# Performance work log

Measured on AMD Instinct MI355X. Metric: run time of the kernel, lower is better.

The kernel has to match this reference:

```python
import jax, jax.numpy as jnp
import numpy as np

B, S, E, H = 4, 8192, 512, 8
D = E // H  # head_dim = 64


def setup_inputs() -> dict:
    key = jax.random.key(0)
    ks = jax.random.split(key, 9)
    scale = 1.0 / np.sqrt(E)
    x = jax.random.normal(ks[0], (B, S, E), dtype=jnp.float32)
    # torch nn.Linear convention: y = x @ W.T + b, W has shape (out, in)
    Wp = jax.random.uniform(ks[1], (E, E), jnp.float32, -scale, scale)
    bp = jax.random.uniform(ks[2], (E,), jnp.float32, -scale, scale)
    Wc = jax.random.uniform(ks[3], (E, E), jnp.float32, -scale, scale)
    bc = jax.random.uniform(ks[4], (E,), jnp.float32, -scale, scale)
    Ws = jax.random.uniform(ks[5], (E, E), jnp.float32, -scale, scale)
    bs = jax.random.uniform(ks[6], (E,), jnp.float32, -scale, scale)
    Wo = jax.random.uniform(ks[7], (E, E), jnp.float32, -scale, scale)
    bo = jax.random.uniform(ks[8], (E,), jnp.float32, -scale, scale)
    return {"x": x, "Wp": Wp, "bp": bp, "Wc": Wc, "bc": bc,
            "Ws": Ws, "bs": bs, "Wo": Wo, "bo": bo}


def reference(x, Wp, bp, Wc, bc, Ws, bs, Wo, bo):
    # Faithful to TreeAttention.forward with tree_structure=None (default path).
    # NOTE: original views projections as (B,S,H,D) without transposing head/seq,
    # so the matmuls mix HEADS per token (HxH scores), not tokens.
    b, s, _ = x.shape
    parent = (jnp.einsum('bse,fe->bsf', x, Wp) + bp).reshape(b, s, H, D)
    child = (jnp.einsum('bse,fe->bsf', x, Wc) + bc).reshape(b, s, H, D)
    sibling = (jnp.einsum('bse,fe->bsf', x, Ws) + bs).reshape(b, s, H, D)
    # per-token head-mixing scores: (B, S, H, H)
    scores = jnp.einsum('bshd,bstd->bsht', parent, child) / jnp.sqrt(
        jnp.asarray(D, dtype=x.dtype))
    attention = jax.nn.softmax(scores, axis=-1)
    # dropout is identity in eval mode (reference runs in inference mode)
    out = jnp.einsum('bsht,bstd->bshd', attention, sibling).reshape(b, s, E)
    return jnp.einsum('bse,fe->bsf', out, Wo) + bo
```

## Files before the change

### kernel.cpp

```cpp
#include <hip/hip_runtime.h>
#include <hip/hip_bf16.h>

typedef unsigned short u16;
typedef __attribute__((ext_vector_type(8))) short bf16x8;
typedef __attribute__((ext_vector_type(4))) float f32x4;
typedef __attribute__((ext_vector_type(8))) unsigned short u16x8;

#define GLDS(gp, lp) __builtin_amdgcn_global_load_lds( \
    (const __attribute__((address_space(1))) void*)(gp), \
    (__attribute__((address_space(3))) void*)(lp), 16, 0, 0)

__device__ __forceinline__ u16 f2b(float f) {
  unsigned u = __builtin_bit_cast(unsigned, f);
  return (u16)((u + 0x7fffu + ((u >> 16) & 1u)) >> 16);
}
__device__ __forceinline__ float b2f(u16 s) {
  return __builtin_bit_cast(float, (unsigned)s << 16);
}

#define BARX() do { __builtin_amdgcn_sched_barrier(0); \
  asm volatile("s_barrier" ::: "memory"); \
  __builtin_amdgcn_sched_barrier(0); } while (0)

__global__ __launch_bounds__(256) void convert_k(
    const float* __restrict__ x, const float* __restrict__ Wp,
    const float* __restrict__ Wc, const float* __restrict__ Ws,
    const float* __restrict__ Wo, u16* __restrict__ xb,
    u16* __restrict__ wall, u16* __restrict__ wob)
{
  const long CX = 2097152;
  const long CW = 98304;
  const long CO = 32768;
  const long total = CX + CW + CO;
  for (long i = (long)blockIdx.x * blockDim.x + threadIdx.x; i < total;
       i += (long)gridDim.x * blockDim.x) {
    const float* src; u16* dst;
    if (i < CX) {
      src = x + i * 8; dst = xb + i * 8;
    } else if (i < CX + CW) {
      long e = (i - CX) * 8;
      int n = (int)(e >> 9), k = (int)(e & 511);
      const float* wr = (n < 512)  ? (Wp + (long)n * 512)
                      : (n < 1024) ? (Wc + (long)(n - 512) * 512)
                                   : (Ws + (long)(n - 1024) * 512);
      src = wr + k; dst = wall + e;
    } else {
      long e = (i - CX - CW) * 8; src = Wo + e; dst = wob + e;
    }
    f32x4 v0 = *(const f32x4*)src;
    f32x4 v1 = *(const f32x4*)(src + 4);
    u16x8 o;
    o[0]=f2b(v0[0]); o[1]=f2b(v0[1]); o[2]=f2b(v0[2]); o[3]=f2b(v0[3]);
    o[4]=f2b(v1[0]); o[5]=f2b(v1[1]); o[6]=f2b(v1[2]); o[7]=f2b(v1[3]);
    *(u16x8*)dst = o;
  }
}

template<int NC, bool BF16OUT>
__global__ __launch_bounds__(512, 2) void gemm8(
    const u16* __restrict__ A, const u16* __restrict__ Bw,
    const float* __restrict__ bias0, const float* __restrict__ bias1,
    const float* __restrict__ bias2, void* __restrict__ Cout)
{
  __shared__ alignas(16) char smem[131072];
  char* sAc = smem;
  char* sBc = smem + 65536;

  const int tid = threadIdx.x;
  const int w = tid >> 6, lane = tid & 63;
  const int wr = w >> 2, wc = w & 3;
  const int ln15 = lane & 15, g4 = lane >> 4, l7 = lane & 7;

  const int nbx = NC / 256;
  const int nwg = nbx * 128;
  const int qq = nwg / 8;
  const int flat = blockIdx.x;
  const int swz = (flat & 7) * qq + (flat >> 3);
  const int bx = swz % nbx, by = swz / nbx;
  const long row0 = (long)by * 256;
  const int col0 = bx * 256;

  const int t8 = tid >> 3;
  const int gsw = (tid & 7) ^ (t8 & 7);
  const u16* pA = A + (row0 + t8) * 512 + gsw * 8;
  const u16* pB = Bw + ((long)col0 + (t8 >> 5) * 64 + (t8 & 31)) * 512 + gsw * 8;

#define STG_A(bb, h, t) do { \
    const u16* s_ = pA + (h) * 32768 + (t) * 64; \
    char* d_ = sAc + (bb) * 32768 + (h) * 16384 + w * 1024; \
    GLDS(s_, d_); GLDS(s_ + 65536, d_ + 8192); \
  } while (0)
#define STG_B(bb, h, t) do { \
    const u16* s_ = pB + (h) * 16384 + (t) * 64; \
    char* d_ = sBc + (bb) * 32768 + (h) * 16384 + w * 1024; \
    GLDS(s_, d_); GLDS(s_ + 65536, d_ + 8192); \
  } while (0)

  const int gkb0 = (g4 ^ l7) << 4;
  const int gkb1 = ((g4 + 4) ^ l7) << 4;
  const int aoff = (wr * 64 + ln15) * 128;
  const int boff = (wc * 32 + ln15) * 128;

#define LOAD_A(bb, MH) do { \
    const char* ba_ = sAc + (bb) * 32768 + (MH) * 16384 + aoff; \
    _Pragma("unroll") for (int mf = 0; mf < 4; ++mf) { \
      aF[mf][0] = *(const bf16x8*)(ba_ + mf * 2048 + gkb0); \
      aF[mf][1] = *(const bf16x8*)(ba_ + mf * 2048 + gkb1); \
    } } while (0)
#define LOAD_B(bb, NH, BF) do { \
    const char* bb_ = sBc + (bb) * 32768 + (NH) * 16384 + boff; \
    _Pragma("unroll") for (int nf = 0; nf < 2; ++nf) { \
      BF[nf][0] = *(const bf16x8*)(bb_ + nf * 2048 + gkb0); \
      BF[nf][1] = *(const bf16x8*)(bb_ + nf * 2048 + gkb1); \
    } } while (0)
#define MFMA_Q(MH, NH, BF) do { \
    __builtin_amdgcn_s_setprio(1); \
    _Pragma("unroll") for (int mf = 0; mf < 4; ++mf) \
    _Pragma("unroll") for (int nf = 0; nf < 2; ++nf) { \
      f32x4 c_ = acc[(MH) * 4 + mf][(NH) * 2 + nf]; \
      c_ = __builtin_amdgcn_mfma_f32_16x16x32_bf16(aF[mf][0], BF[nf][0], c_, 0, 0, 0); \
      c_ = __builtin_amdgcn_mfma_f32_16x16x32_bf16(aF[mf][1], BF[nf][1], c_, 0, 0, 0); \
      acc[(MH) * 4 + mf][(NH) * 2 + nf] = c_; \
    } \
    __builtin_amdgcn_s_setprio(0); \
  } while (0)
#define WAITB(nstr) do { \
    asm volatile("s_waitcnt vmcnt(" nstr ")" ::: "memory"); BARX(); } while (0)

  f32x4 acc[8][4] = {};

  STG_A(0, 0, 0); STG_B(0, 0, 0); STG_B(0, 1, 0); STG_A(0, 1, 0);
  STG_A(1, 0, 1); STG_B(1, 0, 1); STG_B(1, 1, 1);
  WAITB("10");

#pragma unroll
  for (int it = 0; it < 4; ++it) {
    const int t0 = 2 * it, t1 = t0 + 1;
    const bool st = (it < 3);
    bf16x8 aF[4][2], bFa[2][2], bFb[2][2];

    LOAD_A(0, 0); LOAD_B(0, 0, bFa);
    STG_A(1, 1, t1);
    MFMA_Q(0, 0, bFa);
    if (st) WAITB("10"); else WAITB("2");
    LOAD_B(0, 1, bFb);
    if (st) STG_A(0, 0, t0 + 2);
    MFMA_Q(0, 1, bFb);
    if (st) WAITB("10"); else WAITB("2");
    LOAD_A(0, 1);
    if (st) STG_B(0, 0, t0 + 2);
    MFMA_Q(1, 1, bFb);
    if (st) WAITB("10"); else WAITB("2");
    if (st) STG_B(0, 1, t0 + 2);
    MFMA_Q(1, 0, bFa);
    if (st) WAITB("10"); else WAITB("2");
    LOAD_A(1, 0); LOAD_B(1, 0, bFa);
    if (st) STG_A(0, 1, t0 + 2);
    MFMA_Q(0, 0, bFa);
    if (st) WAITB("10"); else WAITB("2");
    LOAD_B(1, 1, bFb);
    if (st) STG_A(1, 0, t1 + 2);
    MFMA_Q(0, 1, bFb);
    if (st) WAITB("10"); else WAITB("0");
    LOAD_A(1, 1);
    if (st) STG_B(1, 0, t1 + 2);
    MFMA_Q(1, 1, bFb);
    if (st) WAITB("10"); else WAITB("0");
    if (st) STG_B(1, 1, t1 + 2);
    MFMA_Q(1, 0, bFa);
    if (st) WAITB("10"); else WAITB("0");
  }

  __syncthreads();
  const long rgb = row0 + wr * 128;
  const int cgb = col0 + wc * 64;
  if (BF16OUT) {
    u16* sc = (u16*)(smem + (w << 14));
#pragma unroll
    for (int n = 0; n < 4; ++n) {
      const int colg = cgb + ln15 + n * 16;
      const float* bp_ = (NC == 512) ? bias0
                         : (colg < 512 ? bias0 : (colg < 1024 ? bias1 : bias2));
      const float bv = bp_[colg & 511];
      const int c = ln15 + n * 16;
      const int gsl = c >> 3, co = c & 7;
#pragma unroll
      for (int mi = 0; mi < 8; ++mi)
#pragma unroll
        for (int j = 0; j < 4; ++j) {
          const int r = mi * 16 + (g4 << 2) + j;
          sc[r * 64 + (((gsl ^ (r & 7)) << 3) | co)] = f2b(acc[mi][n][j] + bv);
        }
    }
    asm volatile("s_waitcnt lgkmcnt(0)" ::: "memory");
    __builtin_amdgcn_sched_barrier(0);
#pragma unroll
    for (int it = 0; it < 16; ++it) {
      const int rr = it * 8 + (lane >> 3);
      const int gl = lane & 7;
      u16x8 v = *(const u16x8*)(sc + rr * 64 + ((gl ^ (rr & 7)) << 3));
      *(u16x8*)((u16*)Cout + (rgb + rr) * NC + cgb + gl * 8) = v;
    }
  } else {
    float* scf = (float*)(smem + (w << 14));
#pragma unroll
    for (int h = 0; h < 2; ++h) {
#pragma unroll
      for (int n = 0; n < 4; ++n) {
        const int colg = cgb + ln15 + n * 16;
        const float bv = bias0[colg & 511];
        const int c = ln15 + n * 16;
        const int gsl = c >> 2, co = c & 3;
#pragma unroll
        for (int mf = 0; mf < 4; ++mf)
#pragma unroll
          for (int j = 0; j < 4; ++j) {
            const int r = mf * 16 + (g4 << 2) + j;
            scf[r * 64 + (((gsl ^ (r & 7)) << 2) | co)] = acc[h * 4 + mf][n][j] + bv;
          }
      }
      asm volatile("s_waitcnt lgkmcnt(0)" ::: "memory");
      __builtin_amdgcn_sched_barrier(0);
#pragma unroll
      for (int it = 0; it < 16; ++it) {
        const int rr = it * 4 + (lane >> 4);
        const int gl = lane & 15;
        f32x4 v = *(const f32x4*)(scf + rr * 64 + ((gl ^ (rr & 7)) << 2));
        *(f32x4*)((float*)Cout + (rgb + h * 64 + rr) * NC + cgb + gl * 4) = v;
      }
      asm volatile("s_waitcnt lgkmcnt(0)" ::: "memory");
      __builtin_amdgcn_sched_barrier(0);
    }
  }
#undef STG_A
#undef STG_B
#undef LOAD_A
#undef LOAD_B
#undef MFMA_Q
#undef WAITB
}

__global__ __launch_bounds__(256) void attn_k(const u16* __restrict__ PCS,
                                              u16* __restrict__ OUT)
{
  __shared__ float L[4][1664];
  const int w = threadIdx.x >> 6, lane = threadIdx.x & 63;
  const long token = (long)blockIdx.x * 4 + w;
  float* Lw = L[w];
  const int C0 = 544, S0 = 1088, AT0 = 1600;
  const u16* rowp = PCS + token * 1536;
#pragma unroll
  for (int q = 0; q < 3; ++q) {
    u16x8 v = *(const u16x8*)(rowp + q * 512 + lane * 8);
    float* dst = (q < 2) ? (Lw + q * 544 + (lane >> 3) * 68 + (lane & 7) * 8)
                         : (Lw + S0 + lane * 8);
    f32x4 a = {b2f(v[0]), b2f(v[1]), b2f(v[2]), b2f(v[3])};
    f32x4 b = {b2f(v[4]), b2f(v[5]), b2f(v[6]), b2f(v[7])};
    *(f32x4*)dst = a;
    *(f32x4*)(dst + 4) = b;
  }
  const int h = lane >> 3, t = lane & 7;
  float sc = 0.f;
#pragma unroll
  for (int d = 0; d < 64; d += 4) {
    f32x4 pv = *(const f32x4*)(Lw + h * 68 + d);
    f32x4 cv = *(const f32x4*)(Lw + C0 + t * 68 + d);
    sc += pv[0]*cv[0] + pv[1]*cv[1] + pv[2]*cv[2] + pv[3]*cv[3];
  }
  sc *= 0.125f;
  float mx = sc;
  mx = fmaxf(mx, __shfl_xor(mx, 1));
  mx = fmaxf(mx, __shfl_xor(mx, 2));
  mx = fmaxf(mx, __shfl_xor(mx, 4));
  float e = __expf(sc - mx);
  float sm = e;
  sm += __shfl_xor(sm, 1);
  sm += __shfl_xor(sm, 2);
  sm += __shfl_xor(sm, 4);
  Lw[AT0 + lane] = e / sm;
  float o[8] = {0, 0, 0, 0, 0, 0, 0, 0};
#pragma unroll
  for (int tt = 0; tt < 8; ++tt) {
    const float av = Lw[AT0 + h * 8 + tt];
    f32x4 s0 = *(const f32x4*)(Lw + S0 + tt * 64 + t * 8);
    f32x4 s1 = *(const f32x4*)(Lw + S0 + tt * 64 + t * 8 + 4);
    o[0] += av * s0[0]; o[1] += av * s0[1]; o[2] += av * s0[2]; o[3] += av * s0[3];
    o[4] += av * s1[0]; o[5] += av * s1[1]; o[6] += av * s1[2]; o[7] += av * s1[3];
  }
  u16x8 ov;
#pragma unroll
  for (int j = 0; j < 8; ++j) ov[j] = f2b(o[j]);
  *(u16x8*)(OUT + token * 512 + lane * 8) = ov;
}

extern "C" void kernel_launch(void* const* d_in, const int* in_sizes, int n_in,
                              void* d_out, int out_size, void* d_ws, size_t ws_size,
                              hipStream_t stream) {
  const float* x  = (const float*)d_in[0];
  const float* Wp = (const float*)d_in[1];
  const float* bp = (const float*)d_in[2];
  const float* Wc = (const float*)d_in[3];
  const float* bc = (const float*)d_in[4];
  const float* Ws = (const float*)d_in[5];
  const float* bs = (const float*)d_in[6];
  const float* Wo = (const float*)d_in[7];
  const float* bo = (const float*)d_in[8];

  char* ws = (char*)d_ws;
  u16* xb   = (u16*)ws;
  u16* wall = (u16*)(ws + 33554432);
  u16* wob  = (u16*)(ws + 35127296);
  u16* pcs  = (u16*)(ws + 35651584);
  u16* outb = xb;

  convert_k<<<2048, 256, 0, stream>>>(x, Wp, Wc, Ws, Wo, xb, wall, wob);
  gemm8<1536, true><<<768, 512, 0, stream>>>(xb, wall, bp, bc, bs, pcs);
  attn_k<<<8192, 256, 0, stream>>>(pcs, outb);
  gemm8<512, false><<<256, 512, 0, stream>>>(outb, wob, bo, bo, bo, d_out);
}
```

Baseline: 136.5 us.

## Halve GEMM LDS to single-buffered stages with in-place refill pipeline

Shrinks the GEMM's shared memory from 128KB to 64KB by dropping the double-buffered K stage and refilling each A/B half in place right after it is consumed, with a rewritten wait/barrier schedule. The epilogue is split into smaller row chunks so it fits the smaller per-wave scratch area. The intent is to allow two 512-thread workgroups per CU, matching the launch bounds, so memory latency is hidden by occupancy rather than by buffering. The trade-off is less prefetch distance inside each block and more barriers per K step.

```diff
diff --git a/kernel.cpp b/kernel.cpp
--- a/kernel.cpp
+++ b/kernel.cpp
@@ -62,9 +62,9 @@
     const float* __restrict__ bias0, const float* __restrict__ bias1,
     const float* __restrict__ bias2, void* __restrict__ Cout)
 {
-  __shared__ alignas(16) char smem[131072];
+  __shared__ alignas(16) char smem[65536];
   char* sAc = smem;
-  char* sBc = smem + 65536;
+  char* sBc = smem + 32768;
 
   const int tid = threadIdx.x;
   const int w = tid >> 6, lane = tid & 63;
@@ -85,14 +85,14 @@
   const u16* pA = A + (row0 + t8) * 512 + gsw * 8;
   const u16* pB = Bw + ((long)col0 + (t8 >> 5) * 64 + (t8 & 31)) * 512 + gsw * 8;
 
-#define STG_A(bb, h, t) do { \
+#define STG_A(h, t) do { \
     const u16* s_ = pA + (h) * 32768 + (t) * 64; \
-    char* d_ = sAc + (bb) * 32768 + (h) * 16384 + w * 1024; \
+    char* d_ = sAc + (h) * 16384 + w * 1024; \
     GLDS(s_, d_); GLDS(s_ + 65536, d_ + 8192); \
   } while (0)
-#define STG_B(bb, h, t) do { \
+#define STG_B(h, t) do { \
     const u16* s_ = pB + (h) * 16384 + (t) * 64; \
-    char* d_ = sBc + (bb) * 32768 + (h) * 16384 + w * 1024; \
+    char* d_ = sBc + (h) * 16384 + w * 1024; \
     GLDS(s_, d_); GLDS(s_ + 65536, d_ + 8192); \
   } while (0)
 
@@ -101,14 +101,14 @@
   const int aoff = (wr * 64 + ln15) * 128;
   const int boff = (wc * 32 + ln15) * 128;
 
-#define LOAD_A(bb, MH) do { \
-    const char* ba_ = sAc + (bb) * 32768 + (MH) * 16384 + aoff; \
+#define LOAD_A(MH) do { \
+    const char* ba_ = sAc + (MH) * 16384 + aoff; \
     _Pragma("unroll") for (int mf = 0; mf < 4; ++mf) { \
       aF[mf][0] = *(const bf16x8*)(ba_ + mf * 2048 + gkb0); \
       aF[mf][1] = *(const bf16x8*)(ba_ + mf * 2048 + gkb1); \
     } } while (0)
-#define LOAD_B(bb, NH, BF) do { \
-    const char* bb_ = sBc + (bb) * 32768 + (NH) * 16384 + boff; \
+#define LOAD_B(NH, BF) do { \
+    const char* bb_ = sBc + (NH) * 16384 + boff; \
     _Pragma("unroll") for (int nf = 0; nf < 2; ++nf) { \
       BF[nf][0] = *(const bf16x8*)(bb_ + nf * 2048 + gkb0); \
       BF[nf][1] = *(const bf16x8*)(bb_ + nf * 2048 + gkb1); \
@@ -124,87 +124,72 @@
     } \
     __builtin_amdgcn_s_setprio(0); \
   } while (0)
-#define WAITB(nstr) do { \
-    asm volatile("s_waitcnt vmcnt(" nstr ")" ::: "memory"); BARX(); } while (0)
+#define VMW(nstr) asm volatile("s_waitcnt vmcnt(" nstr ")" ::: "memory")
 
   f32x4 acc[8][4] = {};
 
-  STG_A(0, 0, 0); STG_B(0, 0, 0); STG_B(0, 1, 0); STG_A(0, 1, 0);
-  STG_A(1, 0, 1); STG_B(1, 0, 1); STG_B(1, 1, 1);
-  WAITB("10");
-
-#pragma unroll
-  for (int it = 0; it < 4; ++it) {
-    const int t0 = 2 * it, t1 = t0 + 1;
-    const bool st = (it < 3);
+  STG_A(0, 0); STG_B(0, 0); STG_B(1, 0); STG_A(1, 0);
+
+  for (int t = 0; t < 8; ++t) {
+    const bool st = (t < 7);
     bf16x8 aF[4][2], bFa[2][2], bFb[2][2];
 
-    LOAD_A(0, 0); LOAD_B(0, 0, bFa);
-    STG_A(1, 1, t1);
+    VMW("4"); BARX();
+    LOAD_A(0); LOAD_B(0, bFa);
     MFMA_Q(0, 0, bFa);
-    if (st) WAITB("10"); else WAITB("2");
-    LOAD_B(0, 1, bFb);
-    if (st) STG_A(0, 0, t0 + 2);
+    VMW("2"); BARX();
+    if (st) { STG_A(0, t + 1); STG_B(0, t + 1); }
+    LOAD_B(1, bFb);
     MFMA_Q(0, 1, bFb);
-    if (st) WAITB("10"); else WAITB("2");
-    LOAD_A(0, 1);
-    if (st) STG_B(0, 0, t0 + 2);
+    if (st) VMW("4"); else VMW("0");
+    BARX();
+    if (st) STG_B(1, t + 1);
+    LOAD_A(1);
     MFMA_Q(1, 1, bFb);
-    if (st) WAITB("10"); else WAITB("2");
-    if (st) STG_B(0, 1, t0 + 2);
+    BARX();
+    if (st) STG_A(1, t + 1);
     MFMA_Q(1, 0, bFa);
-    if (st) WAITB("10"); else WAITB("2");
-    LOAD_A(1, 0); LOAD_B(1, 0, bFa);
-    if (st) STG_A(0, 1, t0 + 2);
-    MFMA_Q(0, 0, bFa);
-    if (st) WAITB("10"); else WAITB("2");
-    LOAD_B(1, 1, bFb);
-    if (st) STG_A(1, 0, t1 + 2);
-    MFMA_Q(0, 1, bFb);
-    if (st) WAITB("10"); else WAITB("0");
-    LOAD_A(1, 1);
-    if (st) STG_B(1, 0, t1 + 2);
-    MFMA_Q(1, 1, bFb);
-    if (st) WAITB("10"); else WAITB("0");
-    if (st) STG_B(1, 1, t1 + 2);
-    MFMA_Q(1, 0, bFa);
-    if (st) WAITB("10"); else WAITB("0");
   }
 
   __syncthreads();
   const long rgb = row0 + wr * 128;
   const int cgb = col0 + wc * 64;
   if (BF16OUT) {
-    u16* sc = (u16*)(smem + (w << 14));
-#pragma unroll
-    for (int n = 0; n < 4; ++n) {
-      const int colg = cgb + ln15 + n * 16;
-      const float* bp_ = (NC == 512) ? bias0
-                         : (colg < 512 ? bias0 : (colg < 1024 ? bias1 : bias2));
-      const float bv = bp_[colg & 511];
-      const int c = ln15 + n * 16;
-      const int gsl = c >> 3, co = c & 7;
-#pragma unroll
-      for (int mi = 0; mi < 8; ++mi)
-#pragma unroll
-        for (int j = 0; j < 4; ++j) {
-          const int r = mi * 16 + (g4 << 2) + j;
-          sc[r * 64 + (((gsl ^ (r & 7)) << 3) | co)] = f2b(acc[mi][n][j] + bv);
-        }
-    }
-    asm volatile("s_waitcnt lgkmcnt(0)" ::: "memory");
-    __builtin_amdgcn_sched_barrier(0);
-#pragma unroll
-    for (int it = 0; it < 16; ++it) {
-      const int rr = it * 8 + (lane >> 3);
-      const int gl = lane & 7;
-      u16x8 v = *(const u16x8*)(sc + rr * 64 + ((gl ^ (rr & 7)) << 3));
-      *(u16x8*)((u16*)Cout + (rgb + rr) * NC + cgb + gl * 8) = v;
+    u16* sc = (u16*)(smem + (w << 13));
+#pragma unroll
+    for (int h2 = 0; h2 < 2; ++h2) {
+#pragma unroll
+      for (int n = 0; n < 4; ++n) {
+        const int colg = cgb + ln15 + n * 16;
+        const float* bp_ = (NC == 512) ? bias0
+                           : (colg < 512 ? bias0 : (colg < 1024 ? bias1 : bias2));
+        const float bv = bp_[colg & 511];
+        const int c = ln15 + n * 16;
+        const int gsl = c >> 3, co = c & 7;
+#pragma unroll
+        for (int mf = 0; mf < 4; ++mf)
+#pragma unroll
+          for (int j = 0; j < 4; ++j) {
+            const int r = mf * 16 + (g4 << 2) + j;
+            sc[r * 64 + (((gsl ^ (r & 7)) << 3) | co)] = f2b(acc[h2 * 4 + mf][n][j] + bv);
+          }
+      }
+      asm volatile("s_waitcnt lgkmcnt(0)" ::: "memory");
+      __builtin_amdgcn_sched_barrier(0);
+#pragma unroll
+      for (int it = 0; it < 8; ++it) {
+        const int rr = it * 8 + (lane >> 3);
+        const int gl = lane & 7;
+        u16x8 v = *(const u16x8*)(sc + rr * 64 + ((gl ^ (rr & 7)) << 3));
+        *(u16x8*)((u16*)Cout + (rgb + h2 * 64 + rr) * NC + cgb + gl * 8) = v;
+      }
+      asm volatile("s_waitcnt lgkmcnt(0)" ::: "memory");
+      __builtin_amdgcn_sched_barrier(0);
     }
   } else {
-    float* scf = (float*)(smem + (w << 14));
-#pragma unroll
-    for (int h = 0; h < 2; ++h) {
+    float* scf = (float*)(smem + (w << 13));
+#pragma unroll
+    for (int q = 0; q < 4; ++q) {
 #pragma unroll
       for (int n = 0; n < 4; ++n) {
         const int colg = cgb + ln15 + n * 16;
@@ -212,21 +197,21 @@
         const int c = ln15 + n * 16;
         const int gsl = c >> 2, co = c & 3;
 #pragma unroll
-        for (int mf = 0; mf < 4; ++mf)
+        for (int mh = 0; mh < 2; ++mh)
 #pragma unroll
           for (int j = 0; j < 4; ++j) {
-            const int r = mf * 16 + (g4 << 2) + j;
-            scf[r * 64 + (((gsl ^ (r & 7)) << 2) | co)] = acc[h * 4 + mf][n][j] + bv;
+            const int r = mh * 16 + (g4 << 2) + j;
+            scf[r * 64 + (((gsl ^ (r & 7)) << 2) | co)] = acc[q * 2 + mh][n][j] + bv;
           }
       }
       asm volatile("s_waitcnt lgkmcnt(0)" ::: "memory");
       __builtin_amdgcn_sched_barrier(0);
 #pragma unroll
-      for (int it = 0; it < 16; ++it) {
+      for (int it = 0; it < 8; ++it) {
         const int rr = it * 4 + (lane >> 4);
         const int gl = lane & 15;
         f32x4 v = *(const f32x4*)(scf + rr * 64 + ((gl ^ (rr & 7)) << 2));
-        *(f32x4*)((float*)Cout + (rgb + h * 64 + rr) * NC + cgb + gl * 4) = v;
+        *(f32x4*)((float*)Cout + (rgb + q * 32 + rr) * NC + cgb + gl * 4) = v;
       }
       asm volatile("s_waitcnt lgkmcnt(0)" ::: "memory");
       __builtin_amdgcn_sched_barrier(0);
@@ -237,7 +222,7 @@
 #undef LOAD_A
 #undef LOAD_B
 #undef MFMA_Q
-#undef WAITB
+#undef VMW
 }
 
 __global__ __launch_bounds__(256) void attn_k(const u16* __restrict__ PCS,
```

New measurement: 133.2 us. -2.4%, faster.
